# Kernel optimization log

Hardware: AMD Instinct MI355X
Metric: run time of the kernel (lower is better)

## Reference

```python
import jax, jax.numpy as jnp
import numpy as np

N, DIN, DH, DOUT, E, K = 8192, 1024, 4096, 1024, 8, 2
AUX_EPS = 1e-10


def setup_inputs() -> dict:
    key = jax.random.key(0)
    kx, kgw, kgb, kw1, kb1, kw2, kb2 = jax.random.split(key, 7)
    def init(k, shape, fan_in):
        return (jax.random.normal(k, shape, jnp.float32) / np.sqrt(fan_in)).astype(jnp.float32)
    return {
        "x": jax.random.normal(kx, (N, DIN), jnp.float32),
        "gate_w": init(kgw, (DIN, E), DIN),
        "gate_b": jnp.zeros((E,), jnp.float32),
        "w1": init(kw1, (E, DIN, DH), DIN),
        "b1": jnp.zeros((E, DH), jnp.float32),
        "w2": init(kw2, (E, DH, DOUT), DH),
        "b2": jnp.zeros((E, DOUT), jnp.float32),
    }


def reference(x, gate_w, gate_b, w1, b1, w2, b2):
    # Gating
    logits = x @ gate_w + gate_b                      # [N, E]
    probs = jax.nn.softmax(logits, axis=-1)           # [N, E]
    topk_vals, topk_idx = jax.lax.top_k(probs, K)     # [N, K]
    topk_norm = topk_vals / (topk_vals.sum(-1, keepdims=True) + AUX_EPS)

    # Scatter normalized top-k weights into a dense [N, E] combine matrix.
    n = x.shape[0]
    weights = jnp.zeros((n, E), x.dtype).at[jnp.arange(n)[:, None], topk_idx].add(topk_norm)

    # Dense all-expert FFN (same math: non-selected experts get weight 0).
    h = jax.nn.relu(jnp.einsum('nd,edh->neh', x, w1) + b1)   # [N, E, DH]
    y = jnp.einsum('neh,eho->neo', h, w2) + b2               # [N, E, DOUT]
    output = jnp.einsum('neo,ne->no', y, weights)            # [N, DOUT]

    # Aux load-balancing loss: KL(mean_probs || uniform)
    mean_probs = probs.mean(axis=0)
    aux_loss = jnp.sum(mean_probs * jnp.log(mean_probs * E + AUX_EPS))

    return output, aux_loss, probs
```

## Files before the change

### kernel.cpp

```cpp
#include <hip/hip_runtime.h>

#define NTOK 8192
#define DIN 1024
#define DH   4096
#define DOUT 1024
#define NE   8
#define MAXTILES 136
#define SLOTCAP  (MAXTILES*128)

typedef __bf16 bf16x8 __attribute__((ext_vector_type(8)));
typedef float  f32x4  __attribute__((ext_vector_type(4)));

constexpr size_t OFF_W1T  = 0;
constexpr size_t OFF_W2T  = 67108864;
constexpr size_t OFF_XB   = 134217728;
constexpr size_t OFF_H    = 150994944;
constexpr size_t OFF_SROW = 293601280;
constexpr size_t OFF_SW   = 293670912;
constexpr size_t OFF_TIDX = 293740544;
constexpr size_t OFF_TW   = 293806080;
constexpr size_t OFF_CTRL = 293871616;
constexpr size_t OFF_PART = 293871744;

__device__ __forceinline__ ushort f2bf(float f){
  unsigned u = __float_as_uint(f);
  u += 0x7fff + ((u >> 16) & 1);
  return (ushort)(u >> 16);
}

#define GLDS(g,l) __builtin_amdgcn_global_load_lds( \
    (const __attribute__((address_space(1))) void*)(g), \
    (__attribute__((address_space(3))) void*)(l), 16, 0, 0)

__global__ void k_cvt_x(const float4* __restrict__ x, ushort4* __restrict__ xb){
  int i = blockIdx.x * 256 + threadIdx.x;
  float4 v = x[i];
  ushort4 o;
  o.x = f2bf(v.x); o.y = f2bf(v.y); o.z = f2bf(v.z); o.w = f2bf(v.w);
  xb[i] = o;
}

__global__ void k_transpose(const float* __restrict__ W, ushort* __restrict__ WT, int R, int C){
  __shared__ ushort tl[64][65];
  int e  = blockIdx.z;
  int r0 = blockIdx.x * 64, c0 = blockIdx.y * 64;
  const float* Wp  = W  + (size_t)e * R * C;
  ushort*      WTp = WT + (size_t)e * R * C;
  int tr = threadIdx.x >> 6, tc = threadIdx.x & 63;
#pragma unroll
  for (int i = 0; i < 16; i++){
    int r = tr + i * 4;
    tl[r][tc] = f2bf(Wp[(size_t)(r0 + r) * C + c0 + tc]);
  }
  __syncthreads();
#pragma unroll
  for (int i = 0; i < 16; i++){
    int r = tr + i * 4;
    WTp[(size_t)(c0 + r) * R + r0 + tc] = tl[tc][r];
  }
}

__global__ void k_gate(const float* __restrict__ x, const float* __restrict__ gw,
                       const float* __restrict__ gb, float* __restrict__ probs_out,
                       int* __restrict__ topk_idx, float* __restrict__ topk_w,
                       int* __restrict__ count, float* __restrict__ partial){
  __shared__ float psum[8];
  __shared__ int   pcnt[8];
  int wv = threadIdx.x >> 6, lane = threadIdx.x & 63;
  int row = blockIdx.x * 4 + wv;
  if (threadIdx.x < 8){ psum[threadIdx.x] = 0.f; pcnt[threadIdx.x] = 0; }
  __syncthreads();

  const float4* x4 = (const float4*)(x + (size_t)row * DIN);
  float acc[8];
#pragma unroll
  for (int e = 0; e < 8; e++) acc[e] = 0.f;
#pragma unroll
  for (int j = 0; j < 4; j++){
    float4 v = x4[j * 64 + lane];
    int kbase = (j * 64 + lane) * 4;
#pragma unroll
    for (int c = 0; c < 4; c++){
      float xv = (&v.x)[c];
      const float4* g4 = (const float4*)(gw + (size_t)(kbase + c) * 8);
      float4 g0 = g4[0], g1 = g4[1];
      acc[0] += xv * g0.x; acc[1] += xv * g0.y; acc[2] += xv * g0.z; acc[3] += xv * g0.w;
      acc[4] += xv * g1.x; acc[5] += xv * g1.y; acc[6] += xv * g1.z; acc[7] += xv * g1.w;
    }
  }
#pragma unroll
  for (int e = 0; e < 8; e++)
#pragma unroll
    for (int off = 32; off; off >>= 1) acc[e] += __shfl_xor(acc[e], off, 64);

  float lg[8], p[8], mx = -1e30f, s = 0.f;
#pragma unroll
  for (int e = 0; e < 8; e++){ lg[e] = acc[e] + gb[e]; mx = fmaxf(mx, lg[e]); }
#pragma unroll
  for (int e = 0; e < 8; e++){ p[e] = expf(lg[e] - mx); s += p[e]; }
  float inv = 1.f / s;
#pragma unroll
  for (int e = 0; e < 8; e++) p[e] *= inv;

  if (lane < 8) probs_out[(size_t)row * 8 + lane] = p[lane];

  if (lane == 0){
    int i1 = 0; float v1 = p[0];
#pragma unroll
    for (int e = 1; e < 8; e++) if (p[e] > v1){ v1 = p[e]; i1 = e; }
    int i2 = -1; float v2 = -1.f;
#pragma unroll
    for (int e = 0; e < 8; e++){ if (e == i1) continue; if (p[e] > v2){ v2 = p[e]; i2 = e; } }
    float denom = 1.f / (v1 + v2 + 1e-10f);
    topk_idx[row * 2]     = i1;  topk_idx[row * 2 + 1] = i2;
    topk_w  [row * 2]     = v1 * denom;  topk_w[row * 2 + 1] = v2 * denom;
    atomicAdd(&pcnt[i1], 1); atomicAdd(&pcnt[i2], 1);
  }
  if (lane < 8) atomicAdd(&psum[lane], p[lane]);
  __syncthreads();
  if (threadIdx.x < 8){
    partial[(size_t)blockIdx.x * 8 + threadIdx.x] = psum[threadIdx.x];
    if (pcnt[threadIdx.x]) atomicAdd(&count[threadIdx.x], pcnt[threadIdx.x]);
  }
}

__global__ void k_aux(const float* __restrict__ partial, const int* __restrict__ count,
                      float* __restrict__ aux_out, int* __restrict__ tile_off){
  __shared__ float red[256];
  __shared__ float tot[8];
  int t = threadIdx.x, e = t & 7;
  float s = 0.f;
  for (int b = (t >> 3); b < 2048; b += 32) s += partial[(size_t)b * 8 + e];
  red[t] = s; __syncthreads();
  if (t < 8){ float v = 0.f; for (int c = 0; c < 32; c++) v += red[c * 8 + t]; tot[t] = v; }
  __syncthreads();
  if (t == 0){
    float aux = 0.f;
    for (int i = 0; i < 8; i++){
      float m = tot[i] * (1.f / 8192.f);
      aux += m * logf(m * 8.f + 1e-10f);
    }
    aux_out[0] = aux;
    int off = 0;
    for (int i = 0; i < 8; i++){ tile_off[i] = off; off += (count[i] + 127) >> 7; }
    tile_off[8] = off;
  }
}

__global__ void k_scatter(const int* __restrict__ topk_idx, const float* __restrict__ topk_w,
                          const int* __restrict__ tile_off, int* __restrict__ fill,
                          int* __restrict__ slot_row, float* __restrict__ slot_w){
  int i = blockIdx.x * 256 + threadIdx.x;
  int row = i >> 1;
  int e = topk_idx[i];
  float w = topk_w[i];
  int lane = threadIdx.x & 63;
  int pos = 0;
#pragma unroll
  for (int ex = 0; ex < 8; ex++){
    unsigned long long mask = __ballot(e == ex);
    if (e == ex){
      int leader = __ffsll((long long)mask) - 1;
      int base = 0;
      if (lane == leader) base = atomicAdd(&fill[ex], (int)__popcll(mask));
      base = __shfl(base, leader, 64);
      pos = base + (int)__popcll(mask & ((1ull << lane) - 1ull));
    }
  }
  int slot = tile_off[e] * 128 + pos;
  slot_row[slot] = row;
  slot_w[slot]   = w;
}

__global__ __launch_bounds__(256) void k_gemm1(
    const ushort* __restrict__ xb, const ushort* __restrict__ w1t,
    const float* __restrict__ b1, const int* __restrict__ slot_row,
    const int* __restrict__ tile_off, ushort* __restrict__ H){
  __shared__ ushort As[128 * 32];
  __shared__ ushort Bs[128 * 32];
  int tileM = blockIdx.x, tileN = blockIdx.y;
  if (tileM >= tile_off[8]) return;
  int e = 0;
  while (e < 7 && tile_off[e + 1] <= tileM) e++;
  int m0 = tileM * 128, n0 = tileN * 128;
  int t = threadIdx.x;

  const ushort* aBase[2]; const ushort* bBase[2];
#pragma unroll
  for (int i = 0; i < 2; i++){
    int c = i * 256 + t, r = c >> 2, cc = c & 3;
    aBase[i] = xb  + (size_t)slot_row[m0 + r] * DIN + cc * 8;
    bBase[i] = w1t + ((size_t)e * DH + n0 + r) * DIN + cc * 8;
  }
  int wv = t >> 6, lane = t & 63;
  int wm = wv >> 1, wn = wv & 1, quad = lane >> 4, lc = lane & 15;
  f32x4 acc[4][4] = {};

  for (int k0 = 0; k0 < DIN; k0 += 32){
#pragma unroll
    for (int i = 0; i < 2; i++){
      int c = i * 256 + t;
      GLDS(aBase[i] + k0, As + c * 8);
      GLDS(bBase[i] + k0, Bs + c * 8);
    }
    __syncthreads();
    bf16x8 a[4], b[4];
#pragma unroll
    for (int i = 0; i < 4; i++) a[i] = *(const bf16x8*)(As + (wm * 64 + i * 16 + lc) * 32 + quad * 8);
#pragma unroll
    for (int j = 0; j < 4; j++) b[j] = *(const bf16x8*)(Bs + (wn * 64 + j * 16 + lc) * 32 + quad * 8);
#pragma unroll
    for (int i = 0; i < 4; i++)
#pragma unroll
      for (int j = 0; j < 4; j++)
        acc[i][j] = __builtin_amdgcn_mfma_f32_16x16x32_bf16(a[i], b[j], acc[i][j], 0, 0, 0);
    __syncthreads();
  }

  const float* b1e = b1 + (size_t)e * DH;
#pragma unroll
  for (int i = 0; i < 4; i++){
#pragma unroll
    for (int r = 0; r < 4; r++){
      int slot = m0 + wm * 64 + i * 16 + quad * 4 + r;
      ushort* hrow = H + (size_t)slot * DH;
#pragma unroll
      for (int j = 0; j < 4; j++){
        int col = n0 + wn * 64 + j * 16 + lc;
        float v = acc[i][j][r] + b1e[col];
        hrow[col] = f2bf(fmaxf(v, 0.f));
      }
    }
  }
}

__global__ __launch_bounds__(256) void k_gemm2(
    const ushort* __restrict__ H, const ushort* __restrict__ w2t,
    const float* __restrict__ b2, const int* __restrict__ slot_row,
    const float* __restrict__ slot_w, const int* __restrict__ tile_off,
    float* __restrict__ out){
  __shared__ ushort As[128 * 32];
  __shared__ ushort Bs[128 * 32];
  int tileM = blockIdx.x, tileN = blockIdx.y;
  if (tileM >= tile_off[8]) return;
  int e = 0;
  while (e < 7 && tile_off[e + 1] <= tileM) e++;
  int m0 = tileM * 128, n0 = tileN * 128;
  int t = threadIdx.x;

  const ushort* aBase[2]; const ushort* bBase[2];
#pragma unroll
  for (int i = 0; i < 2; i++){
    int c = i * 256 + t, r = c >> 2, cc = c & 3;
    aBase[i] = H   + (size_t)(m0 + r) * DH + cc * 8;
    bBase[i] = w2t + ((size_t)e * DOUT + n0 + r) * DH + cc * 8;
  }
  int wv = t >> 6, lane = t & 63;
  int wm = wv >> 1, wn = wv & 1, quad = lane >> 4, lc = lane & 15;
  f32x4 acc[4][4] = {};

  for (int k0 = 0; k0 < DH; k0 += 32){
#pragma unroll
    for (int i = 0; i < 2; i++){
      int c = i * 256 + t;
      GLDS(aBase[i] + k0, As + c * 8);
      GLDS(bBase[i] + k0, Bs + c * 8);
    }
    __syncthreads();
    bf16x8 a[4], b[4];
#pragma unroll
    for (int i = 0; i < 4; i++) a[i] = *(const bf16x8*)(As + (wm * 64 + i * 16 + lc) * 32 + quad * 8);
#pragma unroll
    for (int j = 0; j < 4; j++) b[j] = *(const bf16x8*)(Bs + (wn * 64 + j * 16 + lc) * 32 + quad * 8);
#pragma unroll
    for (int i = 0; i < 4; i++)
#pragma unroll
      for (int j = 0; j < 4; j++)
        acc[i][j] = __builtin_amdgcn_mfma_f32_16x16x32_bf16(a[i], b[j], acc[i][j], 0, 0, 0);
    __syncthreads();
  }

  const float* b2e = b2 + (size_t)e * DOUT;
#pragma unroll
  for (int i = 0; i < 4; i++){
#pragma unroll
    for (int r = 0; r < 4; r++){
      int slot = m0 + wm * 64 + i * 16 + quad * 4 + r;
      float w = slot_w[slot];
      if (w == 0.f) continue;
      float* orow = out + (size_t)slot_row[slot] * DOUT;
#pragma unroll
      for (int j = 0; j < 4; j++){
        int col = n0 + wn * 64 + j * 16 + lc;
        atomicAdd(orow + col, w * (acc[i][j][r] + b2e[col]));
      }
    }
  }
}

extern "C" void kernel_launch(void* const* d_in, const int* in_sizes, int n_in,
                              void* d_out, int out_size, void* d_ws, size_t ws_size,
                              hipStream_t stream){
  const float* x      = (const float*)d_in[0];
  const float* gate_w = (const float*)d_in[1];
  const float* gate_b = (const float*)d_in[2];
  const float* w1     = (const float*)d_in[3];
  const float* b1     = (const float*)d_in[4];
  const float* w2     = (const float*)d_in[5];
  const float* b2     = (const float*)d_in[6];
  float* out = (float*)d_out;

  char* ws = (char*)d_ws;
  ushort* W1T   = (ushort*)(ws + OFF_W1T);
  ushort* W2T   = (ushort*)(ws + OFF_W2T);
  ushort* XB    = (ushort*)(ws + OFF_XB);
  ushort* H     = (ushort*)(ws + OFF_H);
  int*    SROW  = (int*)   (ws + OFF_SROW);
  float*  SW    = (float*) (ws + OFF_SW);
  int*    TIDX  = (int*)   (ws + OFF_TIDX);
  float*  TW    = (float*) (ws + OFF_TW);
  int*    COUNT = (int*)   (ws + OFF_CTRL);
  int*    FILL  = (int*)   (ws + OFF_CTRL + 32);
  int*    TOFF  = (int*)   (ws + OFF_CTRL + 64);
  float*  PART  = (float*) (ws + OFF_PART);

  float* aux_out   = out + (size_t)NTOK * DOUT;
  float* probs_out = aux_out + 1;

  hipMemsetAsync(d_out, 0, (size_t)out_size * 4, stream);
  hipMemsetAsync(ws + OFF_CTRL, 0, 128, stream);
  hipMemsetAsync(ws + OFF_SROW, 0, (size_t)SLOTCAP * 8, stream);

  k_cvt_x<<<dim3((NTOK * DIN / 4) / 256), 256, 0, stream>>>((const float4*)x, (ushort4*)XB);
  k_transpose<<<dim3(DIN / 64, DH / 64, NE), 256, 0, stream>>>(w1, W1T, DIN, DH);
  k_transpose<<<dim3(DH / 64, DOUT / 64, NE), 256, 0, stream>>>(w2, W2T, DH, DOUT);
  k_gate<<<dim3(NTOK / 4), 256, 0, stream>>>(x, gate_w, gate_b, probs_out, TIDX, TW, COUNT, PART);
  k_aux<<<dim3(1), 256, 0, stream>>>(PART, COUNT, aux_out, TOFF);
  k_scatter<<<dim3(NTOK * 2 / 256), 256, 0, stream>>>(TIDX, TW, TOFF, FILL, SROW, SW);
  k_gemm1<<<dim3(MAXTILES, DH / 128), 256, 0, stream>>>(XB, W1T, b1, SROW, TOFF, H);
  k_gemm2<<<dim3(MAXTILES, DOUT / 128), 256, 0, stream>>>(H, W2T, b2, SROW, SW, TOFF, out);
}
```

Measured before the change: 988.5 us.

## Deepen GEMM K-tile to 64 with XOR-swizzled LDS, grouped block order, vectorized transpose

Both expert GEMMs now stage a K-depth of 64 per iteration instead of 32, halving the number of barrier pairs. An XOR swizzle on the LDS layout avoids bank conflicts on the MFMA fragment reads. The grid is flattened and remapped so that consecutive blocks share A tiles, for better L2 reuse, and launch bounds request 4 blocks per CU. The weight transpose kernel now uses float4 loads and ushort4 stores. LDS use per block doubles, which may limit occupancy.

```diff
diff --git a/kernel.cpp b/kernel.cpp
--- a/kernel.cpp
+++ b/kernel.cpp
@@ -41,22 +41,31 @@
 }
 
 __global__ void k_transpose(const float* __restrict__ W, ushort* __restrict__ WT, int R, int C){
-  __shared__ ushort tl[64][65];
+  __shared__ ushort tl[64][72];
   int e  = blockIdx.z;
   int r0 = blockIdx.x * 64, c0 = blockIdx.y * 64;
   const float* Wp  = W  + (size_t)e * R * C;
   ushort*      WTp = WT + (size_t)e * R * C;
-  int tr = threadIdx.x >> 6, tc = threadIdx.x & 63;
-#pragma unroll
-  for (int i = 0; i < 16; i++){
-    int r = tr + i * 4;
-    tl[r][tc] = f2bf(Wp[(size_t)(r0 + r) * C + c0 + tc]);
+  int t = threadIdx.x;
+  int lr  = t >> 4;
+  int lc4 = t & 15;
+#pragma unroll
+  for (int i = 0; i < 4; i++){
+    int r = lr + i * 16;
+    float4 v = *(const float4*)(Wp + (size_t)(r0 + r) * C + c0 + lc4 * 4);
+    ushort4 o; o.x = f2bf(v.x); o.y = f2bf(v.y); o.z = f2bf(v.z); o.w = f2bf(v.w);
+    *(ushort4*)&tl[r][lc4 * 4] = o;
   }
   __syncthreads();
-#pragma unroll
-  for (int i = 0; i < 16; i++){
-    int r = tr + i * 4;
-    WTp[(size_t)(c0 + r) * R + r0 + tc] = tl[tc][r];
+  int tr4 = t & 15;
+  int tcc = t >> 4;
+#pragma unroll
+  for (int i = 0; i < 4; i++){
+    int c = tcc + i * 16;
+    ushort4 o;
+    o.x = tl[tr4 * 4 + 0][c]; o.y = tl[tr4 * 4 + 1][c];
+    o.z = tl[tr4 * 4 + 2][c]; o.w = tl[tr4 * 4 + 3][c];
+    *(ushort4*)(WTp + (size_t)(c0 + c) * R + r0 + tr4 * 4) = o;
   }
 }
 
@@ -172,48 +181,59 @@
   slot_w[slot]   = w;
 }
 
-__global__ __launch_bounds__(256) void k_gemm1(
+
+__global__ __launch_bounds__(256, 4) void k_gemm1(
     const ushort* __restrict__ xb, const ushort* __restrict__ w1t,
     const float* __restrict__ b1, const int* __restrict__ slot_row,
     const int* __restrict__ tile_off, ushort* __restrict__ H){
-  __shared__ ushort As[128 * 32];
-  __shared__ ushort Bs[128 * 32];
-  int tileM = blockIdx.x, tileN = blockIdx.y;
+  __shared__ ushort As[128 * 64];
+  __shared__ ushort Bs[128 * 64];
+  int id = blockIdx.x;
+  int pid = id >> 8, w = id & 255;
+  int tileN = w & 31;
+  int tileM = pid * 8 + (w >> 5);
   if (tileM >= tile_off[8]) return;
   int e = 0;
   while (e < 7 && tile_off[e + 1] <= tileM) e++;
   int m0 = tileM * 128, n0 = tileN * 128;
   int t = threadIdx.x;
 
-  const ushort* aBase[2]; const ushort* bBase[2];
-#pragma unroll
-  for (int i = 0; i < 2; i++){
-    int c = i * 256 + t, r = c >> 2, cc = c & 3;
-    aBase[i] = xb  + (size_t)slot_row[m0 + r] * DIN + cc * 8;
-    bBase[i] = w1t + ((size_t)e * DH + n0 + r) * DIN + cc * 8;
+  const ushort* aPtr[4]; const ushort* bPtr[4];
+#pragma unroll
+  for (int i = 0; i < 4; i++){
+    int c = i * 256 + t, r = c >> 3, qp = c & 7;
+    int q = qp ^ (r & 7);
+    aPtr[i] = xb  + (size_t)slot_row[m0 + r] * DIN + q * 8;
+    bPtr[i] = w1t + ((size_t)e * DH + n0 + r) * DIN + q * 8;
   }
   int wv = t >> 6, lane = t & 63;
   int wm = wv >> 1, wn = wv & 1, quad = lane >> 4, lc = lane & 15;
   f32x4 acc[4][4] = {};
 
-  for (int k0 = 0; k0 < DIN; k0 += 32){
-#pragma unroll
-    for (int i = 0; i < 2; i++){
+  for (int k0 = 0; k0 < DIN; k0 += 64){
+#pragma unroll
+    for (int i = 0; i < 4; i++){
       int c = i * 256 + t;
-      GLDS(aBase[i] + k0, As + c * 8);
-      GLDS(bBase[i] + k0, Bs + c * 8);
+      GLDS(aPtr[i] + k0, As + c * 8);
+      GLDS(bPtr[i] + k0, Bs + c * 8);
     }
     __syncthreads();
-    bf16x8 a[4], b[4];
-#pragma unroll
-    for (int i = 0; i < 4; i++) a[i] = *(const bf16x8*)(As + (wm * 64 + i * 16 + lc) * 32 + quad * 8);
-#pragma unroll
-    for (int j = 0; j < 4; j++) b[j] = *(const bf16x8*)(Bs + (wn * 64 + j * 16 + lc) * 32 + quad * 8);
-#pragma unroll
-    for (int i = 0; i < 4; i++)
-#pragma unroll
-      for (int j = 0; j < 4; j++)
-        acc[i][j] = __builtin_amdgcn_mfma_f32_16x16x32_bf16(a[i], b[j], acc[i][j], 0, 0, 0);
+#pragma unroll
+    for (int kk = 0; kk < 2; kk++){
+      bf16x8 a[4], b[4];
+#pragma unroll
+      for (int z = 0; z < 4; z++){
+        int ra = wm * 64 + z * 16 + lc;
+        a[z] = *(const bf16x8*)(As + ra * 64 + (((kk * 4 + quad) ^ (ra & 7)) * 8));
+        int rb = wn * 64 + z * 16 + lc;
+        b[z] = *(const bf16x8*)(Bs + rb * 64 + (((kk * 4 + quad) ^ (rb & 7)) * 8));
+      }
+#pragma unroll
+      for (int zi = 0; zi < 4; zi++)
+#pragma unroll
+        for (int zj = 0; zj < 4; zj++)
+          acc[zi][zj] = __builtin_amdgcn_mfma_f32_16x16x32_bf16(a[zi], b[zj], acc[zi][zj], 0, 0, 0);
+    }
     __syncthreads();
   }
 
@@ -234,49 +254,59 @@
   }
 }
 
-__global__ __launch_bounds__(256) void k_gemm2(
+__global__ __launch_bounds__(256, 4) void k_gemm2(
     const ushort* __restrict__ H, const ushort* __restrict__ w2t,
     const float* __restrict__ b2, const int* __restrict__ slot_row,
     const float* __restrict__ slot_w, const int* __restrict__ tile_off,
     float* __restrict__ out){
-  __shared__ ushort As[128 * 32];
-  __shared__ ushort Bs[128 * 32];
-  int tileM = blockIdx.x, tileN = blockIdx.y;
+  __shared__ ushort As[128 * 64];
+  __shared__ ushort Bs[128 * 64];
+  int id = blockIdx.x;
+  int pid = id >> 7, w = id & 127;
+  int tileN = w & 7;
+  int tileM = pid * 16 + (w >> 3);
   if (tileM >= tile_off[8]) return;
   int e = 0;
   while (e < 7 && tile_off[e + 1] <= tileM) e++;
   int m0 = tileM * 128, n0 = tileN * 128;
   int t = threadIdx.x;
 
-  const ushort* aBase[2]; const ushort* bBase[2];
-#pragma unroll
-  for (int i = 0; i < 2; i++){
-    int c = i * 256 + t, r = c >> 2, cc = c & 3;
-    aBase[i] = H   + (size_t)(m0 + r) * DH + cc * 8;
-    bBase[i] = w2t + ((size_t)e * DOUT + n0 + r) * DH + cc * 8;
+  const ushort* aPtr[4]; const ushort* bPtr[4];
+#pragma unroll
+  for (int i = 0; i < 4; i++){
+    int c = i * 256 + t, r = c >> 3, qp = c & 7;
+    int q = qp ^ (r & 7);
+    aPtr[i] = H   + (size_t)(m0 + r) * DH + q * 8;
+    bPtr[i] = w2t + ((size_t)e * DOUT + n0 + r) * DH + q * 8;
   }
   int wv = t >> 6, lane = t & 63;
   int wm = wv >> 1, wn = wv & 1, quad = lane >> 4, lc = lane & 15;
   f32x4 acc[4][4] = {};
 
-  for (int k0 = 0; k0 < DH; k0 += 32){
-#pragma unroll
-    for (int i = 0; i < 2; i++){
+  for (int k0 = 0; k0 < DH; k0 += 64){
+#pragma unroll
+    for (int i = 0; i < 4; i++){
       int c = i * 256 + t;
-      GLDS(aBase[i] + k0, As + c * 8);
-      GLDS(bBase[i] + k0, Bs + c * 8);
+      GLDS(aPtr[i] + k0, As + c * 8);
+      GLDS(bPtr[i] + k0, Bs + c * 8);
     }
     __syncthreads();
-    bf16x8 a[4], b[4];
-#pragma unroll
-    for (int i = 0; i < 4; i++) a[i] = *(const bf16x8*)(As + (wm * 64 + i * 16 + lc) * 32 + quad * 8);
-#pragma unroll
-    for (int j = 0; j < 4; j++) b[j] = *(const bf16x8*)(Bs + (wn * 64 + j * 16 + lc) * 32 + quad * 8);
-#pragma unroll
-    for (int i = 0; i < 4; i++)
-#pragma unroll
-      for (int j = 0; j < 4; j++)
-        acc[i][j] = __builtin_amdgcn_mfma_f32_16x16x32_bf16(a[i], b[j], acc[i][j], 0, 0, 0);
+#pragma unroll
+    for (int kk = 0; kk < 2; kk++){
+      bf16x8 a[4], b[4];
+#pragma unroll
+      for (int z = 0; z < 4; z++){
+        int ra = wm * 64 + z * 16 + lc;
+        a[z] = *(const bf16x8*)(As + ra * 64 + (((kk * 4 + quad) ^ (ra & 7)) * 8));
+        int rb = wn * 64 + z * 16 + lc;
+        b[z] = *(const bf16x8*)(Bs + rb * 64 + (((kk * 4 + quad) ^ (rb & 7)) * 8));
+      }
+#pragma unroll
+      for (int zi = 0; zi < 4; zi++)
+#pragma unroll
+        for (int zj = 0; zj < 4; zj++)
+          acc[zi][zj] = __builtin_amdgcn_mfma_f32_16x16x32_bf16(a[zi], b[zj], acc[zi][zj], 0, 0, 0);
+    }
     __syncthreads();
   }
 
@@ -286,13 +316,13 @@
 #pragma unroll
     for (int r = 0; r < 4; r++){
       int slot = m0 + wm * 64 + i * 16 + quad * 4 + r;
-      float w = slot_w[slot];
-      if (w == 0.f) continue;
+      float w2 = slot_w[slot];
+      if (w2 == 0.f) continue;
       float* orow = out + (size_t)slot_row[slot] * DOUT;
 #pragma unroll
       for (int j = 0; j < 4; j++){
         int col = n0 + wn * 64 + j * 16 + lc;
-        atomicAdd(orow + col, w * (acc[i][j][r] + b2e[col]));
+        atomicAdd(orow + col, w2 * (acc[i][j][r] + b2e[col]));
       }
     }
   }
@@ -337,6 +367,6 @@
   k_gate<<<dim3(NTOK / 4), 256, 0, stream>>>(x, gate_w, gate_b, probs_out, TIDX, TW, COUNT, PART);
   k_aux<<<dim3(1), 256, 0, stream>>>(PART, COUNT, aux_out, TOFF);
   k_scatter<<<dim3(NTOK * 2 / 256), 256, 0, stream>>>(TIDX, TW, TOFF, FILL, SROW, SW);
-  k_gemm1<<<dim3(MAXTILES, DH / 128), 256, 0, stream>>>(XB, W1T, b1, SROW, TOFF, H);
-  k_gemm2<<<dim3(MAXTILES, DOUT / 128), 256, 0, stream>>>(H, W2T, b2, SROW, SW, TOFF, out);
-}
+  k_gemm1<<<dim3(MAXTILES * (DH / 128)), 256, 0, stream>>>(XB, W1T, b1, SROW, TOFF, H);
+  k_gemm2<<<dim3(MAXTILES * (DOUT / 128)), 256, 0, stream>>>(H, W2T, b2, SROW, SW, TOFF, out);
+}
```

New measurement: 1.077 ms. +8.9%, slower.
